# Performance work log

Measured on AMD Instinct MI355X. Metric: run time of the kernel, lower is better.

Reference implementation:

```python
import jax, jax.numpy as jnp
import numpy as np

SIGMA = 0.4  # hp.guided_attention_sigma


def setup_inputs() -> dict:
    key = jax.random.key(0)
    k1, k2, k3 = jax.random.split(key, 3)
    B, T, S = 32, 2048, 512  # batch, trg(mel) len, src(text) len
    source_len = jax.random.randint(k1, (B,), 1, S + 1)
    target_len = jax.random.randint(k2, (B,), 1, T + 1)
    predict_attns = jax.random.uniform(k3, (B, T, S), dtype=jnp.float32)
    return {"source_len": source_len, "target_len": target_len,
            "predict_attns": predict_attns}


def reference(source_len, target_len, predict_attns):
    B, T, S = predict_attns.shape
    # grid_x indexes the output (trg) axis, grid_y the input (src) axis
    x = jnp.arange(T, dtype=jnp.float32)[None, :, None]  # [1,T,1]
    y = jnp.arange(S, dtype=jnp.float32)[None, None, :]  # [1,1,S]
    ilen = source_len.astype(jnp.float32)[:, None, None]  # [B,1,1]
    olen = target_len.astype(jnp.float32)[:, None, None]  # [B,1,1]
    # guided attention weight, zero-padded outside each sample's (olen, ilen) box
    w = 1.0 - jnp.exp(-((y / ilen - x / olen) ** 2) / (2.0 * SIGMA ** 2))
    valid = (x < olen) & (y < ilen)  # [B,T,S] non-pad mask
    w = jnp.where(valid, w, 0.0)
    # masked_select(...).mean(): sum over valid positions / count of valid positions
    num = jnp.sum(w * predict_attns)
    den = jnp.sum(valid).astype(jnp.float32)
    return num / den
```

## Files before the change

kernel.cpp:

```cpp
#include <hip/hip_runtime.h>
#include <hip/hip_bf16.h>


#define GA_T 2048
#define GA_S 512
#define GA_INV2S2 (1.0f / (2.0f * 0.4f * 0.4f))

#define BLOCK 256
#define ROWS_PER_BLOCK 32
#define TILES_X (GA_T / ROWS_PER_BLOCK)
#define NPART (TILES_X * 32)

__global__ __launch_bounds__(BLOCK) void ga_partial_kernel(
    const int* __restrict__ slen, const int* __restrict__ tlen,
    const float* __restrict__ p, float* __restrict__ partial) {
  const int b = blockIdx.y;
  const int t0 = blockIdx.x * ROWS_PER_BLOCK;
  const int bi = b * gridDim.x + blockIdx.x;
  const int ol = tlen[b];

  float acc = 0.0f;

  if (t0 < ol) {
    const int il = slen[b];
    const float inv_il = 1.0f / (float)il;
    const float inv_ol = 1.0f / (float)ol;

    const int r = threadIdx.x >> 7;
    const int sv = threadIdx.x & 127;
    const int s0 = sv << 2;

    if (s0 < il) {
      const float ys0 = (float)(s0 + 0) * inv_il;
      const float ys1 = (float)(s0 + 1) * inv_il;
      const float ys2 = (float)(s0 + 2) * inv_il;
      const float ys3 = (float)(s0 + 3) * inv_il;
      const float m1 = (s0 + 1 < il) ? 1.0f : 0.0f;
      const float m2 = (s0 + 2 < il) ? 1.0f : 0.0f;
      const float m3 = (s0 + 3 < il) ? 1.0f : 0.0f;

      const float* base = p + ((size_t)(b * GA_T + t0 + r) * GA_S + s0);

#pragma unroll
      for (int rr = 0; rr < ROWS_PER_BLOCK; rr += 2) {
        const int t = t0 + rr + r;
        if (t >= ol) break;
        const float4 pv = *reinterpret_cast<const float4*>(base + rr * GA_S);
        const float xo = (float)t * inv_ol;
        float d0 = ys0 - xo, d1 = ys1 - xo, d2 = ys2 - xo, d3 = ys3 - xo;
        float e0 = __expf(-(d0 * d0) * GA_INV2S2);
        float e1 = __expf(-(d1 * d1) * GA_INV2S2);
        float e2 = __expf(-(d2 * d2) * GA_INV2S2);
        float e3 = __expf(-(d3 * d3) * GA_INV2S2);
        float p0 = pv.x, p1 = m1 * pv.y, p2 = m2 * pv.z, p3 = m3 * pv.w;
        acc += p0 - p0 * e0;
        acc += p1 - p1 * e1;
        acc += p2 - p2 * e2;
        acc += p3 - p3 * e3;
      }
    }
  }

  for (int off = 32; off > 0; off >>= 1)
    acc += __shfl_down(acc, off, 64);

  __shared__ float wsum[BLOCK / 64];
  const int lane = threadIdx.x & 63;
  const int wid = threadIdx.x >> 6;
  if (lane == 0) wsum[wid] = acc;
  __syncthreads();

  if (threadIdx.x == 0) {
    partial[bi] = (wsum[0] + wsum[1]) + (wsum[2] + wsum[3]);
  }
}

__global__ __launch_bounds__(64) void ga_final_kernel(
    const int* __restrict__ slen, const int* __restrict__ tlen,
    const float* __restrict__ partial, int B, float* __restrict__ out) {
  const int lane = threadIdx.x;

  double s = 0.0;
#pragma unroll
  for (int k = 0; k < NPART / (64 * 4); ++k) {
    const float4 f =
        *reinterpret_cast<const float4*>(partial + (k * 64 + lane) * 4);
    s += ((double)f.x + (double)f.y) + ((double)f.z + (double)f.w);
  }

  double den = 0.0;
  if (lane < B) den = (double)slen[lane] * (double)tlen[lane];

#pragma unroll
  for (int off = 32; off > 0; off >>= 1) {
    s += __shfl_down(s, off, 64);
    den += __shfl_down(den, off, 64);
  }

  if (lane == 0) out[0] = (float)(s / den);
}

extern "C" void kernel_launch(void* const* d_in, const int* in_sizes, int n_in,
                              void* d_out, int out_size, void* d_ws, size_t ws_size,
                              hipStream_t stream) {
  const int* slen = (const int*)d_in[0];
  const int* tlen = (const int*)d_in[1];
  const float* p = (const float*)d_in[2];
  float* out = (float*)d_out;
  float* partial = (float*)d_ws;

  const int B = in_sizes[0];

  dim3 grid(TILES_X, B);
  ga_partial_kernel<<<grid, BLOCK, 0, stream>>>(slen, tlen, p, partial);
  ga_final_kernel<<<1, 64, 0, stream>>>(slen, tlen, partial, B, out);
}
```

Measured before the change: 16.05 us.

## Load-balance valid work across a flat grid via prefix-sum over samples

Replaces the per-(batch,row-tile) grid with a flat grid of 2048 blocks. Each block computes a prefix sum of valid float4 work items per sample in shared memory and takes an equal contiguous chunk. This removes the load imbalance caused by variable target and source lengths, where many blocks had little or no work and only valid data gets read. In exchange, every item pays a binary search, an integer division and shared-memory lookups, and each block redundantly reads the lengths and builds the prefix.

```diff
diff --git a/kernel.cpp b/kernel.cpp
--- a/kernel.cpp
+++ b/kernel.cpp
@@ -7,58 +7,79 @@
 #define GA_INV2S2 (1.0f / (2.0f * 0.4f * 0.4f))
 
 #define BLOCK 256
-#define ROWS_PER_BLOCK 32
-#define TILES_X (GA_T / ROWS_PER_BLOCK)
-#define NPART (TILES_X * 32)
+#define NBLK 2048
+#define GA_B 32
 
 __global__ __launch_bounds__(BLOCK) void ga_partial_kernel(
     const int* __restrict__ slen, const int* __restrict__ tlen,
     const float* __restrict__ p, float* __restrict__ partial) {
-  const int b = blockIdx.y;
-  const int t0 = blockIdx.x * ROWS_PER_BLOCK;
-  const int bi = b * gridDim.x + blockIdx.x;
-  const int ol = tlen[b];
+  __shared__ unsigned pref[GA_B + 1];
+  __shared__ unsigned Wsh[GA_B];
+  __shared__ int ilsh[GA_B];
+  __shared__ float inv_il_sh[GA_B], inv_ol_sh[GA_B];
+  __shared__ unsigned szsh[GA_B];
+
+  if (threadIdx.x < GA_B) {
+    const int b = threadIdx.x;
+    const int il = slen[b];
+    const int ol = tlen[b];
+    const unsigned W = (unsigned)((il + 3) >> 2);
+    Wsh[b] = W;
+    ilsh[b] = il;
+    inv_il_sh[b] = 1.0f / (float)il;
+    inv_ol_sh[b] = 1.0f / (float)ol;
+    szsh[b] = W * (unsigned)ol;
+  }
+  __syncthreads();
+  if (threadIdx.x == 0) {
+    unsigned run = 0;
+#pragma unroll
+    for (int b = 0; b < GA_B; ++b) { pref[b] = run; run += szsh[b]; }
+    pref[GA_B] = run;
+  }
+  __syncthreads();
+
+  const unsigned S_tot = pref[GA_B];
+  const unsigned chunk = (S_tot + NBLK - 1) / NBLK;
+  const unsigned start = blockIdx.x * chunk;
+  const unsigned end = (start + chunk < S_tot) ? (start + chunk) : S_tot;
 
   float acc = 0.0f;
 
-  if (t0 < ol) {
-    const int il = slen[b];
-    const float inv_il = 1.0f / (float)il;
-    const float inv_ol = 1.0f / (float)ol;
+  for (unsigned q = start + threadIdx.x; q < end; q += BLOCK) {
+    int b = 0;
+#pragma unroll
+    for (int step = 16; step > 0; step >>= 1)
+      if (pref[b + step] <= q) b += step;
 
-    const int r = threadIdx.x >> 7;
-    const int sv = threadIdx.x & 127;
-    const int s0 = sv << 2;
+    const unsigned qr = q - pref[b];
+    const unsigned W = Wsh[b];
+    const unsigned t = qr / W;
+    const unsigned sv = qr - t * W;
+    const int s0 = (int)(sv << 2);
+    const int il = ilsh[b];
+    const float inv_il = inv_il_sh[b];
+    const float xo = (float)t * inv_ol_sh[b];
 
-    if (s0 < il) {
-      const float ys0 = (float)(s0 + 0) * inv_il;
-      const float ys1 = (float)(s0 + 1) * inv_il;
-      const float ys2 = (float)(s0 + 2) * inv_il;
-      const float ys3 = (float)(s0 + 3) * inv_il;
-      const float m1 = (s0 + 1 < il) ? 1.0f : 0.0f;
-      const float m2 = (s0 + 2 < il) ? 1.0f : 0.0f;
-      const float m3 = (s0 + 3 < il) ? 1.0f : 0.0f;
+    const float4 pv = *reinterpret_cast<const float4*>(
+        p + ((size_t)(b * GA_T + (int)t) * GA_S + s0));
 
-      const float* base = p + ((size_t)(b * GA_T + t0 + r) * GA_S + s0);
-
-#pragma unroll
-      for (int rr = 0; rr < ROWS_PER_BLOCK; rr += 2) {
-        const int t = t0 + rr + r;
-        if (t >= ol) break;
-        const float4 pv = *reinterpret_cast<const float4*>(base + rr * GA_S);
-        const float xo = (float)t * inv_ol;
-        float d0 = ys0 - xo, d1 = ys1 - xo, d2 = ys2 - xo, d3 = ys3 - xo;
-        float e0 = __expf(-(d0 * d0) * GA_INV2S2);
-        float e1 = __expf(-(d1 * d1) * GA_INV2S2);
-        float e2 = __expf(-(d2 * d2) * GA_INV2S2);
-        float e3 = __expf(-(d3 * d3) * GA_INV2S2);
-        float p0 = pv.x, p1 = m1 * pv.y, p2 = m2 * pv.z, p3 = m3 * pv.w;
-        acc += p0 - p0 * e0;
-        acc += p1 - p1 * e1;
-        acc += p2 - p2 * e2;
-        acc += p3 - p3 * e3;
-      }
-    }
+    const float d0 = (float)(s0 + 0) * inv_il - xo;
+    const float d1 = (float)(s0 + 1) * inv_il - xo;
+    const float d2 = (float)(s0 + 2) * inv_il - xo;
+    const float d3 = (float)(s0 + 3) * inv_il - xo;
+    const float e0 = __expf(-(d0 * d0) * GA_INV2S2);
+    const float e1 = __expf(-(d1 * d1) * GA_INV2S2);
+    const float e2 = __expf(-(d2 * d2) * GA_INV2S2);
+    const float e3 = __expf(-(d3 * d3) * GA_INV2S2);
+    const float p0 = pv.x;
+    const float p1 = (s0 + 1 < il) ? pv.y : 0.0f;
+    const float p2 = (s0 + 2 < il) ? pv.z : 0.0f;
+    const float p3 = (s0 + 3 < il) ? pv.w : 0.0f;
+    acc += p0 - p0 * e0;
+    acc += p1 - p1 * e1;
+    acc += p2 - p2 * e2;
+    acc += p3 - p3 * e3;
   }
 
   for (int off = 32; off > 0; off >>= 1)
@@ -70,9 +91,8 @@
   if (lane == 0) wsum[wid] = acc;
   __syncthreads();
 
-  if (threadIdx.x == 0) {
-    partial[bi] = (wsum[0] + wsum[1]) + (wsum[2] + wsum[3]);
-  }
+  if (threadIdx.x == 0)
+    partial[blockIdx.x] = (wsum[0] + wsum[1]) + (wsum[2] + wsum[3]);
 }
 
 __global__ __launch_bounds__(64) void ga_final_kernel(
@@ -82,7 +102,7 @@
 
   double s = 0.0;
 #pragma unroll
-  for (int k = 0; k < NPART / (64 * 4); ++k) {
+  for (int k = 0; k < NBLK / (64 * 4); ++k) {
     const float4 f =
         *reinterpret_cast<const float4*>(partial + (k * 64 + lane) * 4);
     s += ((double)f.x + (double)f.y) + ((double)f.z + (double)f.w);
@@ -111,7 +131,6 @@
 
   const int B = in_sizes[0];
 
-  dim3 grid(TILES_X, B);
-  ga_partial_kernel<<<grid, BLOCK, 0, stream>>>(slen, tlen, p, partial);
+  ga_partial_kernel<<<NBLK, BLOCK, 0, stream>>>(slen, tlen, p, partial);
   ga_final_kernel<<<1, 64, 0, stream>>>(slen, tlen, partial, B, out);
 }
```

Result: faster. 14.40 us (-10.3%).
